# Kernel tuning notes

Measured on AMD Instinct MI355X. Metric: run time of the kernel, lower is better.

## Reference

```python
import jax, jax.numpy as jnp
import numpy as np

D = 256   # dim = vis_dim = key_channels = value_channels = audio_dim
BT = 64   # batch*time
H = 64
W = 64
L = 32    # audio length

_CONV_NAMES = ["vis_project", "av", "vv", "vo", "ao", "vs_key", "vs_q1", "vs_q2",
               "as_key", "as_q1", "as_q2", "outconv", "aoc"]


def _conv1(x, w, b):
    # pointwise Conv1d: x [B,C,Lx], w [O,C], b [O]
    return jnp.einsum('oc,bcl->bol', w, x) + b[None, :, None]


def _inorm(x, eps=1e-5):
    # InstanceNorm1d (affine=False): normalize over last (spatial) axis
    m = jnp.mean(x, axis=-1, keepdims=True)
    v = jnp.var(x, axis=-1, keepdims=True)
    return (x - m) * jax.lax.rsqrt(v + eps)


def _gelu(x):
    return jax.nn.gelu(x, approximate=False)


def setup_inputs() -> dict:
    key = jax.random.key(0)
    ks = jax.random.split(key, 40)
    inp = {
        "x": jax.random.normal(ks[0], (BT, D, H, W), jnp.float32),
        "audio": jax.random.normal(ks[1], (BT, D, L), jnp.float32),
        "audio_mask": jnp.ones((BT, L, 1), jnp.float32),
    }
    for i, n in enumerate(_CONV_NAMES):
        inp[n + "_w"] = jax.random.normal(ks[3 + 2 * i], (D, D), jnp.float32) * 0.05
        inp[n + "_b"] = jax.random.normal(ks[4 + 2 * i], (D,), jnp.float32) * 0.01
    inp["gate_w1"] = jax.random.normal(ks[30], (D, D), jnp.float32) * 0.05
    inp["gate_w2"] = jax.random.normal(ks[31], (D, D), jnp.float32) * 0.05
    inp["vis_weight"] = jnp.ones((1,), jnp.float32)
    inp["audio_weight"] = jnp.ones((1,), jnp.float32)
    return inp


def reference(x, audio, audio_mask,
              vis_project_w, vis_project_b, av_w, av_b, vv_w, vv_b, vo_w, vo_b,
              ao_w, ao_b, vs_key_w, vs_key_b, vs_q1_w, vs_q1_b, vs_q2_w, vs_q2_b,
              as_key_w, as_key_b, as_q1_w, as_q1_b, as_q2_w, as_q2_b,
              outconv_w, outconv_b, aoc_w, aoc_b, gate_w1, gate_w2,
              vis_weight, audio_weight):
    bt, c, h, w = x.shape
    hw = h * w
    xf = x.reshape(bt, c, hw)                       # [BT,C,HW] (channels-first tokens)
    scale = float(D) ** -0.5                         # key_channels ** -0.5
    maskT = jnp.swapaxes(audio_mask, 1, 2)           # [BT,1,L]

    # vis_project (Conv1d 1x1 + GELU)
    vis = _gelu(_conv1(xf, vis_project_w, vis_project_b))       # [BT,C,HW]

    # ---- AV_Interaction ----
    audio_value = _conv1(audio, av_w, av_b) * maskT              # [BT,C,L]

    # Visual_Sim (kernel=1 -> unfold is identity)
    q1 = _inorm(_conv1(xf, vs_q1_w, vs_q1_b))                    # [BT,C,HW]
    q = _inorm(_conv1(q1, vs_q2_w, vs_q2_b))                     # [BT,C,HW]
    k = _conv1(audio, vs_key_w, vs_key_b) * maskT                # [BT,C,L]
    sim_v = jnp.einsum('bch,bcl->bhl', q, k) * scale             # [BT,HW,L]
    sim_v = sim_v + (10000.0 * maskT - 10000.0)                  # mask keys
    sim_v = jax.nn.softmax(sim_v, axis=-1)
    vw = jax.nn.softmax(vis_weight)[0]                           # softmax over size-1 -> 1.0
    vis_out = jnp.einsum('bhl,bcl->bhc', sim_v * vw, audio_value)  # [BT,HW,C]
    vis_out = _inorm(_conv1(jnp.swapaxes(vis_out, 1, 2), vo_w, vo_b))  # [BT,C,HW]

    # Audio_Sim (kernel=(1,1) -> pad/unfold identity)
    aq = _conv1(_conv1(audio, as_q1_w, as_q1_b), as_q2_w, as_q2_b)  # [BT,C,L]
    ak = _inorm(_conv1(xf, as_key_w, as_key_b))                     # [BT,C,HW]
    aqT = jnp.swapaxes(aq, 1, 2) * audio_mask                       # [BT,L,C]
    sim_a = jnp.einsum('blc,bch->blh', aqT, ak) * scale             # [BT,L,HW]
    sim_a = sim_a + (10000.0 * audio_mask - 10000.0)                # mask query rows
    sim_a = jax.nn.softmax(sim_a, axis=-1)
    aw = jax.nn.softmax(audio_weight)[0]
    vis_value = _inorm(_conv1(xf, vv_w, vv_b))                      # [BT,C,HW]
    audio_o = jnp.einsum('blh,bch->blc', sim_a * aw, vis_value)     # [BT,L,C]
    audio_res = _conv1(jnp.swapaxes(audio_o, 1, 2), ao_w, ao_b)     # [BT,C,L]

    # ---- Dual fusion: vis * vis_weight_map, out_conv ----
    vis = _gelu(_conv1(vis * vis_out, outconv_w, outconv_b))        # [BT,C,HW]
    vis_res = jnp.swapaxes(vis, 1, 2)                               # [BT,HW,C]

    # ---- DAM block: gated residual + audio residual ----
    gate = jnp.tanh(jax.nn.relu(vis_res @ gate_w1.T) @ gate_w2.T)   # [BT,HW,C]
    x_tok = jnp.swapaxes(xf, 1, 2) + gate * vis_res                 # [BT,HW,C]
    x_out = jnp.swapaxes(x_tok, 1, 2).reshape(bt, c, h, w)
    audio_out = audio + _gelu(_conv1(audio_res, aoc_w, aoc_b))      # [BT,C,L]
    return (x_out, audio_out)
```

## Files before the change

### kernel.cpp

```cpp
#include <hip/hip_runtime.h>
#include <math.h>

#define BT 64
#define CH 256
#define HW 4096
#define AL 32
#define SCALE 0.0625f

typedef unsigned short ushort_t;
typedef __bf16 bf16x8 __attribute__((ext_vector_type(8)));
typedef short  short8 __attribute__((ext_vector_type(8)));
typedef float  f32x4  __attribute__((ext_vector_type(4)));

__device__ __forceinline__ float gelu_f(float x){
    return 0.5f*x*(1.0f+erff(x*0.70710678118654752f));
}
__device__ __forceinline__ ushort_t f2bf(float f){
    unsigned int u = __builtin_bit_cast(unsigned int, f);
    u += 0x7fffu + ((u>>16)&1u);
    return (ushort_t)(u>>16);
}
__device__ __forceinline__ float bf2f(ushort_t h){
    unsigned int u = ((unsigned int)h)<<16;
    return __builtin_bit_cast(float, u);
}

template<int EPI, int TOUT, int WSTAT>
__global__ __launch_bounds__(256,3)
void gemm_mfma_kernel(const ushort_t* __restrict__ Wb, const float* __restrict__ bias,
                      const ushort_t* __restrict__ Xt, float* __restrict__ Out,
                      ushort_t* __restrict__ OutB,
                      const float* __restrict__ E1, const float* __restrict__ E2,
                      float* __restrict__ St)
{
    __shared__ ushort_t sW[2][128*32];
    __shared__ ushort_t sX[2][128*32];
    const int b  = blockIdx.z;
    const int o0 = blockIdx.y*128, p0 = blockIdx.x*128;
    const int tid = threadIdx.x, lane = tid & 63, w = tid >> 6;
    const int wm = w >> 1, wn = w & 1;
    const int rr  = lane >> 2;
    const int csw = ((lane & 3) ^ ((lane >> 3) & 3)) * 8;

    const ushort_t* gwb = Wb + (size_t)(o0 + w*32)*CH;
    const ushort_t* gxb = Xt + ((size_t)b*HW + p0 + w*32)*CH;

    const int rchunk = ((lane >> 4) ^ ((lane >> 1) & 3)) * 8;

    f32x4 acc[4][4] = {};
    f32x4 rw0, rw1, rx0, rx1;

    rw0 = *(const f32x4*)(gwb + (size_t)(  0 + rr)*CH + csw);
    rw1 = *(const f32x4*)(gwb + (size_t)( 16 + rr)*CH + csw);
    rx0 = *(const f32x4*)(gxb + (size_t)(  0 + rr)*CH + csw);
    rx1 = *(const f32x4*)(gxb + (size_t)( 16 + rr)*CH + csw);
    *(f32x4*)(&sW[0][w*1024 +       lane*8]) = rw0;
    *(f32x4*)(&sW[0][w*1024 + 512 + lane*8]) = rw1;
    *(f32x4*)(&sX[0][w*1024 +       lane*8]) = rx0;
    *(f32x4*)(&sX[0][w*1024 + 512 + lane*8]) = rx1;

    int cur = 0;
    for (int t = 0; t < 8; ++t) {
        __syncthreads();

        if (t < 7) {
            const int k0n = (t+1)*32;
            rw0 = *(const f32x4*)(gwb + (size_t)(  0 + rr)*CH + k0n + csw);
            rw1 = *(const f32x4*)(gwb + (size_t)( 16 + rr)*CH + k0n + csw);
            rx0 = *(const f32x4*)(gxb + (size_t)(  0 + rr)*CH + k0n + csw);
            rx1 = *(const f32x4*)(gxb + (size_t)( 16 + rr)*CH + k0n + csw);
        }

        bf16x8 af[4], bfr[4];
        #pragma unroll
        for (int mt = 0; mt < 4; ++mt) {
            short8 raw = *(const short8*)(&sW[cur][(wm*64 + mt*16 + (lane&15))*32 + rchunk]);
            af[mt] = __builtin_bit_cast(bf16x8, raw);
        }
        #pragma unroll
        for (int nt = 0; nt < 4; ++nt) {
            short8 raw = *(const short8*)(&sX[cur][(wn*64 + nt*16 + (lane&15))*32 + rchunk]);
            bfr[nt] = __builtin_bit_cast(bf16x8, raw);
        }
        #pragma unroll
        for (int mt = 0; mt < 4; ++mt)
            #pragma unroll
            for (int nt = 0; nt < 4; ++nt)
                acc[mt][nt] = __builtin_amdgcn_mfma_f32_16x16x32_bf16(af[mt], bfr[nt], acc[mt][nt], 0, 0, 0);

        if (t < 7) {
            const int nxt = cur ^ 1;
            *(f32x4*)(&sW[nxt][w*1024 +       lane*8]) = rw0;
            *(f32x4*)(&sW[nxt][w*1024 + 512 + lane*8]) = rw1;
            *(f32x4*)(&sX[nxt][w*1024 +       lane*8]) = rx0;
            *(f32x4*)(&sX[nxt][w*1024 + 512 + lane*8]) = rx1;
        }
        cur ^= 1;
    }

    const int pcol = lane & 15, quad = lane >> 4;
    const size_t obase = (size_t)b*CH*HW;
    if (TOUT == 0) {
        #pragma unroll
        for (int mt = 0; mt < 4; ++mt) {
            #pragma unroll
            for (int r = 0; r < 4; ++r) {
                const int o = o0 + wm*64 + mt*16 + quad*4 + r;
                const float bv = bias ? bias[o] : 0.0f;
                #pragma unroll
                for (int nt = 0; nt < 4; ++nt) {
                    const int p = p0 + wn*64 + nt*16 + pcol;
                    float v = acc[mt][nt][r] + bv;
                    if (EPI == 1) v = gelu_f(v);
                    if (EPI == 2) v = fmaxf(v, 0.0f);
                    if (EPI == 3) {
                        const size_t idx = obase + (size_t)o*HW + p;
                        v = E1[idx] + tanhf(v)*E2[idx];
                    }
                    Out[obase + (size_t)o*HW + p] = v;
                }
            }
        }
    } else if (TOUT == 1) {
        #pragma unroll
        for (int mt = 0; mt < 4; ++mt) {
            const int ob = o0 + wm*64 + mt*16 + quad*4;
            #pragma unroll
            for (int nt = 0; nt < 4; ++nt) {
                const int p = p0 + wn*64 + nt*16 + pcol;
                ushort4 u;
                float v0 = acc[mt][nt][0] + (bias ? bias[ob+0] : 0.f);
                float v1 = acc[mt][nt][1] + (bias ? bias[ob+1] : 0.f);
                float v2 = acc[mt][nt][2] + (bias ? bias[ob+2] : 0.f);
                float v3 = acc[mt][nt][3] + (bias ? bias[ob+3] : 0.f);
                if (EPI == 1) { v0=gelu_f(v0); v1=gelu_f(v1); v2=gelu_f(v2); v3=gelu_f(v3); }
                if (EPI == 2) { v0=fmaxf(v0,0.f); v1=fmaxf(v1,0.f); v2=fmaxf(v2,0.f); v3=fmaxf(v3,0.f); }
                u.x=f2bf(v0); u.y=f2bf(v1); u.z=f2bf(v2); u.w=f2bf(v3);
                *(ushort4*)(OutB + ((size_t)b*HW + p)*CH + ob) = u;
            }
        }
    } else {
        #pragma unroll
        for (int mt = 0; mt < 4; ++mt) {
            const int ob = o0 + wm*64 + mt*16 + quad*4;
            #pragma unroll
            for (int nt = 0; nt < 4; ++nt) {
                const int p = p0 + wn*64 + nt*16 + pcol;
                float v[4];
                #pragma unroll
                for (int r = 0; r < 4; ++r) {
                    float t = acc[mt][nt][r] + (bias ? bias[ob+r] : 0.f);
                    if (EPI == 1) t = gelu_f(t);
                    if (EPI == 2) t = fmaxf(t, 0.f);
                    v[r] = t;
                    Out[obase + (size_t)(ob+r)*HW + p] = t;
                }
                ushort4 u;
                u.x=f2bf(v[0]); u.y=f2bf(v[1]); u.z=f2bf(v[2]); u.w=f2bf(v[3]);
                *(ushort4*)(OutB + ((size_t)b*HW + p)*CH + ob) = u;
            }
        }
    }

    if (WSTAT) {
        float s1[4][4], s2[4][4];
        #pragma unroll
        for (int mt = 0; mt < 4; ++mt) {
            #pragma unroll
            for (int r = 0; r < 4; ++r) {
                const int o = o0 + wm*64 + mt*16 + quad*4 + r;
                const float bv = bias ? bias[o] : 0.0f;
                float a = 0.f, q = 0.f;
                #pragma unroll
                for (int nt = 0; nt < 4; ++nt) {
                    const float v = acc[mt][nt][r] + bv;
                    a += v; q += v*v;
                }
                #pragma unroll
                for (int off = 1; off < 16; off <<= 1) {
                    a += __shfl_xor(a, off);
                    q += __shfl_xor(q, off);
                }
                s1[mt][r] = a; s2[mt][r] = q;
            }
        }
        float* red = (float*)sW;
        __syncthreads();
        if (wn == 0 && pcol == 0) {
            #pragma unroll
            for (int mt = 0; mt < 4; ++mt)
                #pragma unroll
                for (int r = 0; r < 4; ++r) {
                    const int ol = wm*64 + mt*16 + quad*4 + r;
                    red[ol*2] = s1[mt][r]; red[ol*2+1] = s2[mt][r];
                }
        }
        __syncthreads();
        if (wn == 1 && pcol == 0) {
            #pragma unroll
            for (int mt = 0; mt < 4; ++mt)
                #pragma unroll
                for (int r = 0; r < 4; ++r) {
                    const int ol = wm*64 + mt*16 + quad*4 + r;
                    const int o = o0 + ol;
                    atomicAdd(&St[((size_t)b*CH + o)*2],   red[ol*2]   + s1[mt][r]);
                    atomicAdd(&St[((size_t)b*CH + o)*2+1], red[ol*2+1] + s2[mt][r]);
                }
        }
    }
}

__global__ __launch_bounds__(256)
void zero_kernel(float* __restrict__ p)
{
    p[blockIdx.x*256 + threadIdx.x] = 0.f;
}

__global__ __launch_bounds__(256)
void stats_finalize_kernel(float* __restrict__ St)
{
    const int row = blockIdx.x*256 + threadIdx.x;
    const float s1 = St[(size_t)row*2], s2 = St[(size_t)row*2+1];
    const float mean = s1 * (1.0f/HW);
    const float var  = s2 * (1.0f/HW) - mean*mean;
    St[(size_t)row*2]   = mean;
    St[(size_t)row*2+1] = rsqrtf(var + 1e-5f);
}

template<int MODE>
__global__ __launch_bounds__(256)
void transpose_bf16_kernel(const float* __restrict__ Xa, const ushort_t* __restrict__ Mul,
                           const float* __restrict__ St, ushort_t* __restrict__ Out)
{
    __shared__ float sT[32][33];
    const int b = blockIdx.z, c0 = blockIdx.y*32, p0 = blockIdx.x*32;
    const int tid = threadIdx.x;
    {
        const int cr = tid >> 3, pq = (tid & 7)*4;
        float4 v = *(const float4*)(Xa + ((size_t)b*CH + c0 + cr)*HW + p0 + pq);
        if (MODE >= 1) {
            const float m = St[((size_t)b*CH + c0 + cr)*2];
            const float r = St[((size_t)b*CH + c0 + cr)*2+1];
            v.x = (v.x-m)*r; v.y = (v.y-m)*r; v.z = (v.z-m)*r; v.w = (v.w-m)*r;
        }
        sT[cr][pq+0]=v.x; sT[cr][pq+1]=v.y; sT[cr][pq+2]=v.z; sT[cr][pq+3]=v.w;
    }
    __syncthreads();
    {
        const int pr = tid >> 3, cq = (tid & 7)*4;
        const size_t oidx = ((size_t)b*HW + p0 + pr)*CH + c0 + cq;
        float v0 = sT[cq+0][pr], v1 = sT[cq+1][pr], v2 = sT[cq+2][pr], v3 = sT[cq+3][pr];
        if (MODE == 2) {
            const ushort4 m = *(const ushort4*)(Mul + oidx);
            v0 *= bf2f(m.x); v1 *= bf2f(m.y); v2 *= bf2f(m.z); v3 *= bf2f(m.w);
        }
        ushort4 u; u.x=f2bf(v0); u.y=f2bf(v1); u.z=f2bf(v2); u.w=f2bf(v3);
        *(ushort4*)(Out + oidx) = u;
    }
}

__global__ __launch_bounds__(256)
void wconv_kernel(const float* w0, const float* w1, const float* w2, const float* w3,
                  const float* w4, const float* w5, const float* w6, const float* w7,
                  const float* w8, ushort_t* __restrict__ Wb)
{
    const float* src;
    switch (blockIdx.y) {
        case 0: src=w0; break; case 1: src=w1; break; case 2: src=w2; break;
        case 3: src=w3; break; case 4: src=w4; break; case 5: src=w5; break;
        case 6: src=w6; break; case 7: src=w7; break; default: src=w8; break;
    }
    const int i = (blockIdx.x*256 + threadIdx.x)*4;
    const float4 v = *(const float4*)(src + i);
    ushort4 u; u.x=f2bf(v.x); u.y=f2bf(v.y); u.z=f2bf(v.z); u.w=f2bf(v.w);
    *(ushort4*)(Wb + (size_t)blockIdx.y*65536 + i) = u;
}

template<int EPI, int TR>
__global__ __launch_bounds__(256)
void conv_l_kernel(const float* __restrict__ W, const float* __restrict__ bias,
                   const float* __restrict__ X, float* __restrict__ Out,
                   const float* __restrict__ Mask, const float* __restrict__ Resid,
                   const float* __restrict__ St)
{
    const int b = blockIdx.x;
    const int o = blockIdx.y*8 + (threadIdx.x>>5);
    const int l = threadIdx.x & 31;
    const float* xb = X + (size_t)b*CH*AL + l;
    const float* wr = W + (size_t)o*CH;
    float acc = bias ? bias[o] : 0.0f;
    #pragma unroll 8
    for (int c=0;c<CH;++c) acc = fmaf(wr[c], xb[(size_t)c*AL], acc);
    if (EPI==1) acc *= Mask[b*AL + l];
    if (EPI==4) acc *= Mask[b*AL + l] * St[((size_t)b*CH + o)*2+1] * SCALE;
    if (EPI==2) {
        const size_t oi = (size_t)b*CH*AL + (size_t)o*AL + l;
        acc = Resid[oi] + gelu_f(acc);
    }
    if (TR == 0) Out[(size_t)b*CH*AL + (size_t)o*AL + l] = acc;
    else         Out[((size_t)b*AL + l)*CH + o] = acc;
}

__global__ __launch_bounds__(256)
void lbias_kernel(const float* __restrict__ Kn, const float* __restrict__ St,
                  float* __restrict__ Lb)
{
    const int b = blockIdx.x, tid = threadIdx.x;
    const int l = tid & 31, g = tid >> 5;
    float s = 0.f;
    #pragma unroll 8
    for (int cc=0; cc<32; ++cc){
        const int c = g*32 + cc;
        s += St[((size_t)b*CH + c)*2] * Kn[((size_t)b*CH + c)*AL + l];
    }
    __shared__ float red[8][32];
    red[g][l] = s;
    __syncthreads();
    if (tid < 32){
        float t = 0.f;
        #pragma unroll
        for (int gg=0; gg<8; ++gg) t += red[gg][tid];
        Lb[b*AL + tid] = -t;
    }
}

__global__ __launch_bounds__(256,2)
void attn_v_kernel(const float* __restrict__ Q, const float* __restrict__ Kn,
                   const float* __restrict__ AVt, const float* __restrict__ Lb,
                   const float* __restrict__ Mask, ushort_t* __restrict__ OutB)
{
    __shared__ float smemf[20480];
    float*    sKn  = smemf;
    ushort_t* sOut = (ushort_t*)smemf;
    ushort_t* sPb  = (ushort_t*)(smemf + 8192);
    float*    sAV  = smemf + 12288;

    const int b  = blockIdx.y;
    const int p0 = blockIdx.x * 256;
    const int tid = threadIdx.x, lane = tid & 63, w = tid >> 6;
    const int pg = lane >> 2;
    const int lq = lane & 3;

    #pragma unroll
    for (int ii=0; ii<8; ++ii){
        const int fi = ii*256 + tid;
        *(f32x4*)&sKn[fi*4] = *(const f32x4*)(Kn + (size_t)b*CH*AL + (size_t)fi*4);
        *(f32x4*)&sAV[fi*4] = *(const f32x4*)(AVt + (size_t)b*AL*CH + (size_t)fi*4);
    }
    float bias[8];
    #pragma unroll
    for (int j=0;j<8;++j){
        const int l = lq*8 + j;
        bias[j] = Lb[b*AL + l] + 10000.f*Mask[b*AL + l] - 10000.f;
    }
    __syncthreads();

    const float* Qb = Q + (size_t)b*CH*HW + p0 + w*64 + pg*4;
    float s[4][8] = {};
    {
        f32x4 qa[8], qb2[8];
        #pragma unroll
        for (int kk=0;kk<8;++kk) qa[kk] = *(const f32x4*)(Qb + (size_t)kk*HW);
        for (int kc = 0; kc < 32; kc += 2){
            #pragma unroll
            for (int kk=0;kk<8;++kk) qb2[kk] = *(const f32x4*)(Qb + (size_t)((kc+1)*8+kk)*HW);
            #pragma unroll
            for (int kk=0;kk<8;++kk){
                const int c = kc*8 + kk;
                const f32x4 kn0 = *(const f32x4*)&sKn[c*32 + lq*8];
                const f32x4 kn1 = *(const f32x4*)&sKn[c*32 + lq*8 + 4];
                #pragma unroll
                for (int i=0;i<4;++i){
                    s[i][0]=fmaf(qa[kk][i],kn0[0],s[i][0]); s[i][1]=fmaf(qa[kk][i],kn0[1],s[i][1]);
                    s[i][2]=fmaf(qa[kk][i],kn0[2],s[i][2]); s[i][3]=fmaf(qa[kk][i],kn0[3],s[i][3]);
                    s[i][4]=fmaf(qa[kk][i],kn1[0],s[i][4]); s[i][5]=fmaf(qa[kk][i],kn1[1],s[i][5]);
                    s[i][6]=fmaf(qa[kk][i],kn1[2],s[i][6]); s[i][7]=fmaf(qa[kk][i],kn1[3],s[i][7]);
                }
            }
            if (kc+2 < 32){
                #pragma unroll
                for (int kk=0;kk<8;++kk) qa[kk] = *(const f32x4*)(Qb + (size_t)((kc+2)*8+kk)*HW);
            }
            #pragma unroll
            for (int kk=0;kk<8;++kk){
                const int c = (kc+1)*8 + kk;
                const f32x4 kn0 = *(const f32x4*)&sKn[c*32 + lq*8];
                const f32x4 kn1 = *(const f32x4*)&sKn[c*32 + lq*8 + 4];
                #pragma unroll
                for (int i=0;i<4;++i){
                    s[i][0]=fmaf(qb2[kk][i],kn0[0],s[i][0]); s[i][1]=fmaf(qb2[kk][i],kn0[1],s[i][1]);
                    s[i][2]=fmaf(qb2[kk][i],kn0[2],s[i][2]); s[i][3]=fmaf(qb2[kk][i],kn0[3],s[i][3]);
                    s[i][4]=fmaf(qb2[kk][i],kn1[0],s[i][4]); s[i][5]=fmaf(qb2[kk][i],kn1[1],s[i][5]);
                    s[i][6]=fmaf(qb2[kk][i],kn1[2],s[i][6]); s[i][7]=fmaf(qb2[kk][i],kn1[3],s[i][7]);
                }
            }
        }
    }

    #pragma unroll
    for (int i=0;i<4;++i){
        #pragma unroll
        for (int j=0;j<8;++j) s[i][j] += bias[j];
        float m = s[i][0];
        #pragma unroll
        for (int j=1;j<8;++j) m = fmaxf(m, s[i][j]);
        m = fmaxf(m, __shfl_xor(m, 1));
        m = fmaxf(m, __shfl_xor(m, 2));
        float z = 0.f;
        #pragma unroll
        for (int j=0;j<8;++j){ s[i][j] = expf(s[i][j]-m); z += s[i][j]; }
        z += __shfl_xor(z, 1);
        z += __shfl_xor(z, 2);
        const float rz = 1.f/z;
        #pragma unroll
        for (int j=0;j<8;++j) s[i][j] *= rz;
    }

    {
        const int tok = w*64 + pg*4;
        #pragma unroll
        for (int j=0;j<8;++j){
            const int l = lq*8 + j;
            unsigned u01 = (unsigned)f2bf(s[0][j]) | ((unsigned)f2bf(s[1][j])<<16);
            unsigned u23 = (unsigned)f2bf(s[2][j]) | ((unsigned)f2bf(s[3][j])<<16);
            *(unsigned*)&sPb[l*256 + tok]     = u01;
            *(unsigned*)&sPb[l*256 + tok + 2] = u23;
        }
    }
    __syncthreads();

    const int tokL = tid >> 2;
    const int cq   = tid & 3;
    for (int t0 = 0; t0 < 4; ++t0){
        const int tok = t0*64 + tokL;
        float acc[8][8] = {};
        for (int k=0;k<32;++k){
            const float pv = bf2f(sPb[k*256 + tok]);
            #pragma unroll
            for (int ch=0;ch<8;++ch){
                const f32x4 a0 = *(const f32x4*)&sAV[k*256 + ch*32 + cq*8];
                const f32x4 a1 = *(const f32x4*)&sAV[k*256 + ch*32 + cq*8 + 4];
                acc[ch][0]=fmaf(pv,a0[0],acc[ch][0]); acc[ch][1]=fmaf(pv,a0[1],acc[ch][1]);
                acc[ch][2]=fmaf(pv,a0[2],acc[ch][2]); acc[ch][3]=fmaf(pv,a0[3],acc[ch][3]);
                acc[ch][4]=fmaf(pv,a1[0],acc[ch][4]); acc[ch][5]=fmaf(pv,a1[1],acc[ch][5]);
                acc[ch][6]=fmaf(pv,a1[2],acc[ch][6]); acc[ch][7]=fmaf(pv,a1[3],acc[ch][7]);
            }
        }
        #pragma unroll
        for (int ch=0;ch<8;++ch){
            short8 u;
            #pragma unroll
            for (int j=0;j<8;++j) u[j] = (short)f2bf(acc[ch][j]);
            const int chunk = (ch*4 + cq) ^ (tokL & 7);
            *(short8*)&sOut[tokL*256 + chunk*8] = u;
        }
        __syncthreads();
        {
            ushort_t* Ob = OutB + ((size_t)b*HW + p0 + t0*64)*CH;
            const int chunk = tid & 31;
            #pragma unroll
            for (int ss=0;ss<8;++ss){
                const int row = ss*8 + (tid>>5);
                short8 v = *(const short8*)&sOut[row*256 + ((chunk ^ (row&7))*8)];
                *(short8*)(Ob + (size_t)row*CH + chunk*8) = v;
            }
        }
        __syncthreads();
    }
}

__global__ __launch_bounds__(256)
void sima_raw_kernel(const float* __restrict__ AQ, const float* __restrict__ AK,
                     const float* __restrict__ Mask, const float* __restrict__ St,
                     float* __restrict__ Sraw)
{
    __shared__ float sAQ[CH*AL];
    const int b = blockIdx.y;
    const int p = blockIdx.x*256 + threadIdx.x;
    const int tid = threadIdx.x;
    #pragma unroll
    for (int i=0;i<32;++i){
        const int idx = tid + 256*i;
        sAQ[idx] = AQ[(size_t)b*CH*AL + idx] * Mask[b*AL + (idx&31)] * SCALE
                 * St[((size_t)b*CH + (idx>>5))*2+1];
    }
    __syncthreads();
    float s[32];
    #pragma unroll
    for (int l=0;l<32;++l) s[l]=0.f;
    const float* akb = AK + (size_t)b*CH*HW + p;
    for (int c=0;c<CH;++c){
        const float a = akb[(size_t)c*HW];
        const float* qr = &sAQ[c*32];
        #pragma unroll
        for (int l=0;l<32;++l) s[l] = fmaf(qr[l], a, s[l]);
    }
    float* outp = Sraw + (size_t)b*AL*HW + p;
    #pragma unroll
    for (int l=0;l<32;++l) outp[(size_t)l*HW] = s[l];
}

__global__ __launch_bounds__(256)
void sima_stats_kernel(const float* __restrict__ Sraw, float2* __restrict__ Stats)
{
    const size_t base = (size_t)blockIdx.x * HW;
    const int tid = threadIdx.x;
    float v[16];
    #pragma unroll
    for (int i=0;i<4;++i){
        const float4 t = *(const float4*)(Sraw + base + tid*4 + i*1024);
        v[i*4+0]=t.x; v[i*4+1]=t.y; v[i*4+2]=t.z; v[i*4+3]=t.w;
    }
    float m = v[0];
    #pragma unroll
    for (int i=1;i<16;++i) m = fmaxf(m, v[i]);
    #pragma unroll
    for (int off=1; off<64; off<<=1) m = fmaxf(m, __shfl_xor(m, off));
    __shared__ float rm[4], rz[4];
    if ((tid&63)==0) rm[tid>>6]=m;
    __syncthreads();
    m = fmaxf(fmaxf(rm[0],rm[1]), fmaxf(rm[2],rm[3]));
    float z=0.f;
    #pragma unroll
    for (int i=0;i<16;++i) z += expf(v[i]-m);
    #pragma unroll
    for (int off=1; off<64; off<<=1) z += __shfl_xor(z, off);
    if ((tid&63)==0) rz[tid>>6]=z;
    __syncthreads();
    if (tid==0) Stats[blockIdx.x] = make_float2(m, 1.0f/(rz[0]+rz[1]+rz[2]+rz[3]));
}

__global__ __launch_bounds__(256)
void sima_pv_kernel(const float* __restrict__ Sraw, const float2* __restrict__ SmStats,
                    const float* __restrict__ VV, const float* __restrict__ ChSt,
                    float* __restrict__ AO)
{
    __shared__ float sA[32*33];
    __shared__ float sB[64*36];
    __shared__ float sM[32], sR[32];
    const int b  = blockIdx.x >> 2;
    const int c0 = (blockIdx.x & 3) * 64;
    const int tid = threadIdx.x;
    if (tid < 32){
        const float2 st = SmStats[b*AL + tid];
        sM[tid] = st.x; sR[tid] = st.y;
    }
    __syncthreads();
    const int lh = tid & 15;
    const int cq = tid >> 4;
    const int lr = tid >> 3, k4 = (tid & 7) * 4;
    float acc[2][4] = {{0.f,0.f,0.f,0.f},{0.f,0.f,0.f,0.f}};
    for (int p0=0; p0<HW; p0+=32){
        {
            const float4 t = *(const float4*)(Sraw + ((size_t)b*AL + lr)*HW + p0 + k4);
            const float mm = sM[lr], rr2 = sR[lr];
            sA[lr*33 + k4+0] = expf(t.x-mm)*rr2;
            sA[lr*33 + k4+1] = expf(t.y-mm)*rr2;
            sA[lr*33 + k4+2] = expf(t.z-mm)*rr2;
            sA[lr*33 + k4+3] = expf(t.w-mm)*rr2;
        }
        #pragma unroll
        for (int i=0;i<2;++i){
            const int cc = (tid>>3) + 32*i;
            *(float4*)&sB[cc*36 + k4] = *(const float4*)(VV + ((size_t)b*CH + c0 + cc)*HW + p0 + k4);
        }
        __syncthreads();
        #pragma unroll
        for (int kk=0;kk<32;++kk){
            const float a0 = sA[lh*33 + kk];
            const float a1 = sA[(lh+16)*33 + kk];
            #pragma unroll
            for (int j=0;j<4;++j){
                const float bb = sB[(cq*4+j)*36 + kk];
                acc[0][j] = fmaf(a0, bb, acc[0][j]);
                acc[1][j] = fmaf(a1, bb, acc[1][j]);
            }
        }
        __syncthreads();
    }
    #pragma unroll
    for (int j=0;j<4;++j){
        const int c = c0 + cq*4 + j;
        const float m0 = ChSt[((size_t)b*CH + c)*2];
        const float r0 = ChSt[((size_t)b*CH + c)*2+1];
        AO[((size_t)b*CH + c)*AL + lh]      = (acc[0][j]-m0)*r0;
        AO[((size_t)b*CH + c)*AL + lh + 16] = (acc[1][j]-m0)*r0;
    }
}

extern "C" void kernel_launch(void* const* d_in, const int* in_sizes, int n_in,
                              void* d_out, int out_size, void* d_ws, size_t ws_size,
                              hipStream_t stream)
{
    (void)in_sizes; (void)n_in; (void)out_size; (void)ws_size;
    const float* x     = (const float*)d_in[0];
    const float* audio = (const float*)d_in[1];
    const float* amask = (const float*)d_in[2];
    const float* vis_project_w = (const float*)d_in[3];
    const float* vis_project_b = (const float*)d_in[4];
    const float* av_w = (const float*)d_in[5];
    const float* av_b = (const float*)d_in[6];
    const float* vv_w = (const float*)d_in[7];
    const float* vv_b = (const float*)d_in[8];
    const float* vo_w = (const float*)d_in[9];
    const float* vo_b = (const float*)d_in[10];
    const float* ao_w = (const float*)d_in[11];
    const float* ao_b = (const float*)d_in[12];
    const float* vs_key_w = (const float*)d_in[13];
    const float* vs_key_b = (const float*)d_in[14];
    const float* vs_q1_w = (const float*)d_in[15];
    const float* vs_q1_b = (const float*)d_in[16];
    const float* vs_q2_w = (const float*)d_in[17];
    const float* vs_q2_b = (const float*)d_in[18];
    const float* as_key_w = (const float*)d_in[19];
    const float* as_key_b = (const float*)d_in[20];
    const float* as_q1_w = (const float*)d_in[21];
    const float* as_q1_b = (const float*)d_in[22];
    const float* as_q2_w = (const float*)d_in[23];
    const float* as_q2_b = (const float*)d_in[24];
    const float* outconv_w = (const float*)d_in[25];
    const float* outconv_b = (const float*)d_in[26];
    const float* aoc_w = (const float*)d_in[27];
    const float* aoc_b = (const float*)d_in[28];
    const float* gate_w1 = (const float*)d_in[29];
    const float* gate_w2 = (const float*)d_in[30];

    float* out_x = (float*)d_out;
    float* out_a = out_x + (size_t)BT*CH*HW;
    float* B     = out_x;

    const size_t BIG = (size_t)BT*CH*HW;
    ushort_t* Xt   = (ushort_t*)d_ws;
    ushort_t* VISB = Xt + BIG;
    float*  A     = (float*)(VISB + BIG);
    float*  SIMA  = A + BIG;
    float2* STATS = (float2*)(SIMA + (size_t)BT*AL*HW);
    float*  S0 = (float*)(STATS + BT*AL);
    float*  S1 = S0 + (size_t)BT*CH*AL;
    float*  S2 = S1 + (size_t)BT*CH*AL;
    float*  S3 = S2 + (size_t)BT*CH*AL;
    float*  S4 = S3 + (size_t)BT*CH*AL;
    ushort_t* Wb = (ushort_t*)(S4 + (size_t)BT*CH*AL);
    float*  SA = (float*)(Wb + (size_t)9*65536);
    float*  SB = SA + (size_t)2*BT*CH;
    float*  LB = SB + (size_t)2*BT*CH;

    dim3 b256(256);
    dim3 gW(64, 9);
    dim3 gL(BT, CH/8);
    dim3 gT(HW/32, CH/32, BT);
    dim3 gG(HW/128, CH/128, BT);
    dim3 gAttnV(HW/256, BT);
    dim3 gSimA(HW/256, BT);
    dim3 gZ(2*BT*CH/256);
    dim3 gF(BT*CH/256);

    #define WSLOT(i) (Wb + (size_t)(i)*65536)
    hipLaunchKernelGGL(wconv_kernel, gW, b256, 0, stream,
                       vs_q1_w, as_key_w, vv_w, vis_project_w, vs_q2_w, vo_w, outconv_w, gate_w1, gate_w2, Wb);
    hipLaunchKernelGGL((conv_l_kernel<1,1>), gL, b256, 0, stream, av_w, av_b, audio, S0, amask, nullptr, nullptr);
    hipLaunchKernelGGL((conv_l_kernel<0,0>), gL, b256, 0, stream, as_q1_w, as_q1_b, audio, S3, nullptr, nullptr, nullptr);
    hipLaunchKernelGGL((conv_l_kernel<0,0>), gL, b256, 0, stream, as_q2_w, as_q2_b, S3, S2, nullptr, nullptr, nullptr);
    hipLaunchKernelGGL((transpose_bf16_kernel<0>), gT, b256, 0, stream, x, nullptr, nullptr, Xt);
    hipLaunchKernelGGL(zero_kernel, gZ, b256, 0, stream, SA);
    hipLaunchKernelGGL((gemm_mfma_kernel<0,0,1>), gG, b256, 0, stream, WSLOT(0), vs_q1_b, Xt, A, nullptr, nullptr, nullptr, SA);
    hipLaunchKernelGGL(stats_finalize_kernel, gF, b256, 0, stream, SA);
    hipLaunchKernelGGL(zero_kernel, gZ, b256, 0, stream, SB);
    hipLaunchKernelGGL((gemm_mfma_kernel<0,0,1>), gG, b256, 0, stream, WSLOT(1), as_key_b, Xt, B, nullptr, nullptr, nullptr, SB);
    hipLaunchKernelGGL(stats_finalize_kernel, gF, b256, 0, stream, SB);
    hipLaunchKernelGGL(sima_raw_kernel, gSimA, b256, 0, stream, S2, B, amask, SB, SIMA);
    hipLaunchKernelGGL(sima_stats_kernel, dim3(BT*AL), b256, 0, stream, SIMA, STATS);
    hipLaunchKernelGGL(zero_kernel, gZ, b256, 0, stream, SB);
    hipLaunchKernelGGL((gemm_mfma_kernel<0,0,1>), gG, b256, 0, stream, WSLOT(2), vv_b, Xt, B, nullptr, nullptr, nullptr, SB);
    hipLaunchKernelGGL(stats_finalize_kernel, gF, b256, 0, stream, SB);
    hipLaunchKernelGGL(sima_pv_kernel, dim3(BT*4), b256, 0, stream, SIMA, STATS, B, SB, S4);
    hipLaunchKernelGGL((conv_l_kernel<0,0>), gL, b256, 0, stream, ao_w, ao_b, S4, S3, nullptr, nullptr, nullptr);
    hipLaunchKernelGGL((conv_l_kernel<2,0>), gL, b256, 0, stream, aoc_w, aoc_b, S3, out_a, nullptr, audio, nullptr);
    hipLaunchKernelGGL((gemm_mfma_kernel<1,1,0>), gG, b256, 0, stream, WSLOT(3), vis_project_b, Xt, nullptr, VISB, nullptr, nullptr, nullptr);
    hipLaunchKernelGGL((transpose_bf16_kernel<1>), gT, b256, 0, stream, A, nullptr, SA, Xt);
    hipLaunchKernelGGL(zero_kernel, gZ, b256, 0, stream, SA);
    hipLaunchKernelGGL((gemm_mfma_kernel<0,0,1>), gG, b256, 0, stream, WSLOT(4), vs_q2_b, Xt, B, nullptr, nullptr, nullptr, SA);
    hipLaunchKernelGGL(stats_finalize_kernel, gF, b256, 0, stream, SA);
    hipLaunchKernelGGL((conv_l_kernel<4,0>), gL, b256, 0, stream, vs_key_w, vs_key_b, audio, S1, amask, nullptr, SA);
    hipLaunchKernelGGL(lbias_kernel, dim3(BT), b256, 0, stream, S1, SA, LB);
    hipLaunchKernelGGL(attn_v_kernel, gAttnV, b256, 0, stream, B, S1, S0, LB, amask, Xt);
    hipLaunchKernelGGL(zero_kernel, gZ, b256, 0, stream, SA);
    hipLaunchKernelGGL((gemm_mfma_kernel<0,0,1>), gG, b256, 0, stream, WSLOT(5), vo_b, Xt, B, nullptr, nullptr, nullptr, SA);
    hipLaunchKernelGGL(stats_finalize_kernel, gF, b256, 0, stream, SA);
    hipLaunchKernelGGL((transpose_bf16_kernel<2>), gT, b256, 0, stream, B, VISB, SA, Xt);
    hipLaunchKernelGGL((gemm_mfma_kernel<1,2,0>), gG, b256, 0, stream, WSLOT(6), outconv_b, Xt, A, VISB, nullptr, nullptr, nullptr);
    hipLaunchKernelGGL((gemm_mfma_kernel<2,1,0>), gG, b256, 0, stream, WSLOT(7), nullptr, VISB, nullptr, Xt, nullptr, nullptr, nullptr);
    hipLaunchKernelGGL((gemm_mfma_kernel<3,0,0>), gG, b256, 0, stream, WSLOT(8), nullptr, Xt, out_x, nullptr, x, A, nullptr);
    #undef WSLOT
}
```

Baseline: 2.808 ms.

## Fuse three GEMMs sharing the same input tile into one kernel

Adds a kernel that loads a 128-token tile of the bf16 transposed input into shared memory once, then computes the vs_q1, as_key and vis_project projections from it, each with its own epilogue: stats atomics for the first two and GELU to bf16 for the third. This replaces three separate GEMM launches that each re-read the input from global memory. The generic GEMM grid is also reordered so output-channel blocks vary fastest, which lets neighbouring blocks share input tiles in cache. In exchange the fused kernel uses 64KB+ of shared memory, which lowers occupancy, and it streams the weights without deep pipelining.

```diff
diff --git a/kernel.cpp b/kernel.cpp
--- a/kernel.cpp
+++ b/kernel.cpp
@@ -23,6 +23,169 @@
 __device__ __forceinline__ float bf2f(ushort_t h){
     unsigned int u = ((unsigned int)h)<<16;
     return __builtin_bit_cast(float, u);
+}
+
+template<int MODE>
+__device__ __forceinline__ void fused_head(
+    const ushort_t* __restrict__ Wm, const float* __restrict__ bias,
+    float* __restrict__ OutF, ushort_t* __restrict__ OutBf, float* __restrict__ St,
+    ushort_t* sXp, ushort_t* sWd0, ushort_t* sWd1,
+    int b, int p0, int tid)
+{
+    const int lane = tid & 63, w = tid >> 6;
+    const int wm = w >> 1, wn = w & 1;
+    const int rr  = lane >> 2;
+    const int csw = ((lane & 3) ^ ((lane >> 3) & 3)) * 8;
+    const int rchunk = ((lane >> 4) ^ ((lane >> 1) & 3)) * 8;
+    const int pcol = lane & 15, quad = lane >> 4;
+    const size_t obase = (size_t)b*CH*HW;
+
+    #pragma unroll 1
+    for (int oh = 0; oh < 2; ++oh) {
+        const int o0 = oh*128;
+        const ushort_t* gwb = Wm + (size_t)(o0 + w*32)*CH;
+        f32x4 acc[4][4] = {};
+        f32x4 rw0 = *(const f32x4*)(gwb + (size_t)(     rr)*CH + csw);
+        f32x4 rw1 = *(const f32x4*)(gwb + (size_t)(16 + rr)*CH + csw);
+
+        for (int t = 0; t < 8; ++t) {
+            __syncthreads();
+            ushort_t* sw = (t & 1) ? sWd1 : sWd0;
+            *(f32x4*)(&sw[w*1024 +       lane*8]) = rw0;
+            *(f32x4*)(&sw[w*1024 + 512 + lane*8]) = rw1;
+            if (t < 7) {
+                rw0 = *(const f32x4*)(gwb + (size_t)(     rr)*CH + (t+1)*32 + csw);
+                rw1 = *(const f32x4*)(gwb + (size_t)(16 + rr)*CH + (t+1)*32 + csw);
+            }
+            __syncthreads();
+
+            bf16x8 af[4], bfr[4];
+            #pragma unroll
+            for (int mt = 0; mt < 4; ++mt) {
+                short8 raw = *(const short8*)(&sw[(wm*64 + mt*16 + (lane&15))*32 + rchunk]);
+                af[mt] = __builtin_bit_cast(bf16x8, raw);
+            }
+            #pragma unroll
+            for (int nt = 0; nt < 4; ++nt) {
+                const int prow = wn*64 + nt*16 + (lane&15);
+                const int u = (t*4 + (lane>>4)) ^ (prow & 7);
+                short8 raw = *(const short8*)(&sXp[prow*256 + u*8]);
+                bfr[nt] = __builtin_bit_cast(bf16x8, raw);
+            }
+            #pragma unroll
+            for (int mt = 0; mt < 4; ++mt)
+                #pragma unroll
+                for (int nt = 0; nt < 4; ++nt)
+                    acc[mt][nt] = __builtin_amdgcn_mfma_f32_16x16x32_bf16(af[mt], bfr[nt], acc[mt][nt], 0, 0, 0);
+        }
+
+        if (MODE == 0) {
+            #pragma unroll
+            for (int mt = 0; mt < 4; ++mt) {
+                #pragma unroll
+                for (int r = 0; r < 4; ++r) {
+                    const int o = o0 + wm*64 + mt*16 + quad*4 + r;
+                    const float bv = bias[o];
+                    #pragma unroll
+                    for (int nt = 0; nt < 4; ++nt) {
+                        const int p = p0 + wn*64 + nt*16 + pcol;
+                        OutF[obase + (size_t)o*HW + p] = acc[mt][nt][r] + bv;
+                    }
+                }
+            }
+            float s1[4][4], s2[4][4];
+            #pragma unroll
+            for (int mt = 0; mt < 4; ++mt) {
+                #pragma unroll
+                for (int r = 0; r < 4; ++r) {
+                    const int o = o0 + wm*64 + mt*16 + quad*4 + r;
+                    const float bv = bias[o];
+                    float a = 0.f, q = 0.f;
+                    #pragma unroll
+                    for (int nt = 0; nt < 4; ++nt) {
+                        const float v = acc[mt][nt][r] + bv;
+                        a += v; q += v*v;
+                    }
+                    #pragma unroll
+                    for (int off = 1; off < 16; off <<= 1) {
+                        a += __shfl_xor(a, off);
+                        q += __shfl_xor(q, off);
+                    }
+                    s1[mt][r] = a; s2[mt][r] = q;
+                }
+            }
+            float* red = (float*)sWd0;
+            __syncthreads();
+            if (wn == 0 && pcol == 0) {
+                #pragma unroll
+                for (int mt = 0; mt < 4; ++mt)
+                    #pragma unroll
+                    for (int r = 0; r < 4; ++r) {
+                        const int ol = wm*64 + mt*16 + quad*4 + r;
+                        red[ol*2] = s1[mt][r]; red[ol*2+1] = s2[mt][r];
+                    }
+            }
+            __syncthreads();
+            if (wn == 1 && pcol == 0) {
+                #pragma unroll
+                for (int mt = 0; mt < 4; ++mt)
+                    #pragma unroll
+                    for (int r = 0; r < 4; ++r) {
+                        const int ol = wm*64 + mt*16 + quad*4 + r;
+                        const int o = o0 + ol;
+                        atomicAdd(&St[((size_t)b*CH + o)*2],   red[ol*2]   + s1[mt][r]);
+                        atomicAdd(&St[((size_t)b*CH + o)*2+1], red[ol*2+1] + s2[mt][r]);
+                    }
+            }
+        } else {
+            #pragma unroll
+            for (int mt = 0; mt < 4; ++mt) {
+                const int ob = o0 + wm*64 + mt*16 + quad*4;
+                #pragma unroll
+                for (int nt = 0; nt < 4; ++nt) {
+                    const int p = p0 + wn*64 + nt*16 + pcol;
+                    ushort4 u;
+                    u.x = f2bf(gelu_f(acc[mt][nt][0] + bias[ob+0]));
+                    u.y = f2bf(gelu_f(acc[mt][nt][1] + bias[ob+1]));
+                    u.z = f2bf(gelu_f(acc[mt][nt][2] + bias[ob+2]));
+                    u.w = f2bf(gelu_f(acc[mt][nt][3] + bias[ob+3]));
+                    *(ushort4*)(OutBf + ((size_t)b*HW + p)*CH + ob) = u;
+                }
+            }
+        }
+    }
+}
+
+__global__ __launch_bounds__(256,2)
+void gemm3_fused_kernel(const ushort_t* __restrict__ W0, const float* __restrict__ b0,
+                        const ushort_t* __restrict__ W1, const float* __restrict__ b1,
+                        const ushort_t* __restrict__ W2, const float* __restrict__ b2,
+                        const ushort_t* __restrict__ Xt,
+                        float* __restrict__ Out0, float* __restrict__ Out1,
+                        ushort_t* __restrict__ OutV,
+                        float* __restrict__ St0, float* __restrict__ St1)
+{
+    __shared__ ushort_t sXp[128*256];
+    __shared__ ushort_t sWdA[128*32];
+    __shared__ ushort_t sWdB[128*32];
+    const int b  = blockIdx.y;
+    const int p0 = blockIdx.x * 128;
+    const int tid = threadIdx.x;
+
+    {
+        const int u = tid & 31;
+        const int rbase = tid >> 5;
+        #pragma unroll
+        for (int i = 0; i < 16; ++i) {
+            const int r = rbase + i*8;
+            f32x4 v = *(const f32x4*)(Xt + ((size_t)b*HW + p0 + r)*CH + u*8);
+            *(f32x4*)(&sXp[r*256 + ((u ^ (r & 7))*8)]) = v;
+        }
+    }
+
+    fused_head<0>(W0, b0, Out0, nullptr, St0, sXp, sWdA, sWdB, b, p0, tid);
+    fused_head<0>(W1, b1, Out1, nullptr, St1, sXp, sWdA, sWdB, b, p0, tid);
+    fused_head<1>(W2, b2, nullptr, OutV, nullptr, sXp, sWdA, sWdB, b, p0, tid);
 }
 
 template<int EPI, int TOUT, int WSTAT>
@@ -36,7 +199,7 @@
     __shared__ ushort_t sW[2][128*32];
     __shared__ ushort_t sX[2][128*32];
     const int b  = blockIdx.z;
-    const int o0 = blockIdx.y*128, p0 = blockIdx.x*128;
+    const int o0 = blockIdx.x*128, p0 = blockIdx.y*128;
     const int tid = threadIdx.x, lane = tid & 63, w = tid >> 6;
     const int wm = w >> 1, wn = w & 1;
     const int rr  = lane >> 2;
@@ -649,7 +812,8 @@
     dim3 gW(64, 9);
     dim3 gL(BT, CH/8);
     dim3 gT(HW/32, CH/32, BT);
-    dim3 gG(HW/128, CH/128, BT);
+    dim3 gG(CH/128, HW/128, BT);
+    dim3 gF3(HW/128, BT);
     dim3 gAttnV(HW/256, BT);
     dim3 gSimA(HW/256, BT);
     dim3 gZ(2*BT*CH/256);
@@ -663,10 +827,11 @@
     hipLaunchKernelGGL((conv_l_kernel<0,0>), gL, b256, 0, stream, as_q2_w, as_q2_b, S3, S2, nullptr, nullptr, nullptr);
     hipLaunchKernelGGL((transpose_bf16_kernel<0>), gT, b256, 0, stream, x, nullptr, nullptr, Xt);
     hipLaunchKernelGGL(zero_kernel, gZ, b256, 0, stream, SA);
-    hipLaunchKernelGGL((gemm_mfma_kernel<0,0,1>), gG, b256, 0, stream, WSLOT(0), vs_q1_b, Xt, A, nullptr, nullptr, nullptr, SA);
+    hipLaunchKernelGGL(zero_kernel, gZ, b256, 0, stream, SB);
+    hipLaunchKernelGGL(gemm3_fused_kernel, gF3, b256, 0, stream,
+                       WSLOT(0), vs_q1_b, WSLOT(1), as_key_b, WSLOT(3), vis_project_b,
+                       Xt, A, B, VISB, SA, SB);
     hipLaunchKernelGGL(stats_finalize_kernel, gF, b256, 0, stream, SA);
-    hipLaunchKernelGGL(zero_kernel, gZ, b256, 0, stream, SB);
-    hipLaunchKernelGGL((gemm_mfma_kernel<0,0,1>), gG, b256, 0, stream, WSLOT(1), as_key_b, Xt, B, nullptr, nullptr, nullptr, SB);
     hipLaunchKernelGGL(stats_finalize_kernel, gF, b256, 0, stream, SB);
     hipLaunchKernelGGL(sima_raw_kernel, gSimA, b256, 0, stream, S2, B, amask, SB, SIMA);
     hipLaunchKernelGGL(sima_stats_kernel, dim3(BT*AL), b256, 0, stream, SIMA, STATS);
@@ -676,7 +841,6 @@
     hipLaunchKernelGGL(sima_pv_kernel, dim3(BT*4), b256, 0, stream, SIMA, STATS, B, SB, S4);
     hipLaunchKernelGGL((conv_l_kernel<0,0>), gL, b256, 0, stream, ao_w, ao_b, S4, S3, nullptr, nullptr, nullptr);
     hipLaunchKernelGGL((conv_l_kernel<2,0>), gL, b256, 0, stream, aoc_w, aoc_b, S3, out_a, nullptr, audio, nullptr);
-    hipLaunchKernelGGL((gemm_mfma_kernel<1,1,0>), gG, b256, 0, stream, WSLOT(3), vis_project_b, Xt, nullptr, VISB, nullptr, nullptr, nullptr);
     hipLaunchKernelGGL((transpose_bf16_kernel<1>), gT, b256, 0, stream, A, nullptr, SA, Xt);
     hipLaunchKernelGGL(zero_kernel, gZ, b256, 0, stream, SA);
     hipLaunchKernelGGL((gemm_mfma_kernel<0,0,1>), gG, b256, 0, stream, WSLOT(4), vs_q2_b, Xt, B, nullptr, nullptr, nullptr, SA);
```

Measured after the change: 2.882 ms. +2.6%, slower.
